# Performance work log

Hardware: AMD Instinct MI355X
Metric: run time of the kernel (lower is better)

The kernel has to match this reference:

```python
import jax, jax.numpy as jnp
import numpy as np

EPS = 1e-8


def setup_inputs() -> dict:
    key = jax.random.key(0)
    k1, k2 = jax.random.split(key)
    N, D = 4096, 512
    x = jax.random.normal(k1, (N, D, 1, 1), dtype=jnp.float32)
    y = jax.random.normal(k2, (N, D, 1, 1), dtype=jnp.float32)
    return {"x": x, "y": y}


def reference(x, y):
    # squeeze trailing singleton spatial dims -> (N, D)
    xs = x[:, :, 0, 0]
    ys = y[:, :, 0, 0]
    # cosine similarity = normalize-then-GEMM (avoids (N,N,D) broadcast intermediate)
    xn = xs / jnp.maximum(jnp.linalg.norm(xs, axis=-1, keepdims=True), EPS)
    yn = ys / jnp.maximum(jnp.linalg.norm(ys, axis=-1, keepdims=True), EPS)
    sim = jnp.einsum("nd,md->nm", xn, yn)  # (N, N)
    n = sim.shape[0]
    # zero the diagonal, then mean over all N*N entries
    sim = sim * (1.0 - jnp.eye(n, dtype=sim.dtype))
    return jnp.mean(sim)
```

## Files before the change

kernel.cpp:

```cpp
#include <hip/hip_runtime.h>

#define NROWS 4096
#define DCOLS 512
#define NBLK  256
#define RBLK  64
#define EPSF 1e-8f
#define MAGICV 0x3C96A5D2u

__device__ __forceinline__ void st_agent(float* p, float v) {
    __hip_atomic_store(p, v, __ATOMIC_RELAXED, __HIP_MEMORY_SCOPE_AGENT);
}
__device__ __forceinline__ float ld_agent(const float* p) {
    return __hip_atomic_load(p, __ATOMIC_RELAXED, __HIP_MEMORY_SCOPE_AGENT);
}
__device__ __forceinline__ void st_flag(unsigned* p, unsigned v) {
    __hip_atomic_store(p, v, __ATOMIC_RELAXED, __HIP_MEMORY_SCOPE_AGENT);
}
__device__ __forceinline__ unsigned ld_flag(const unsigned* p) {
    return __hip_atomic_load(p, __ATOMIC_RELAXED, __HIP_MEMORY_SCOPE_AGENT);
}

__global__ __launch_bounds__(512) void cosloss_fused(const float4* __restrict__ x4,
                                                     const float4* __restrict__ y4,
                                                     float* __restrict__ partx,
                                                     float* __restrict__ party,
                                                     float* __restrict__ partd,
                                                     float* __restrict__ blockpart,
                                                     unsigned* __restrict__ flags,
                                                     unsigned* __restrict__ flag2,
                                                     float* __restrict__ out) {
    __shared__ float4 sx4[8][128];
    __shared__ float4 sy4[8][128];
    __shared__ float ldsd[8];
    __shared__ float ldsx[8][8];
    __shared__ float ldsy[8][8];

    const int t    = threadIdx.x;
    const int lane = t & 63;
    const int wave = t >> 6;

    {
        const int row0 = blockIdx.x * 16 + wave * 2;
        float4 psx0 = {0.f,0.f,0.f,0.f}, psx1 = {0.f,0.f,0.f,0.f};
        float4 psy0 = {0.f,0.f,0.f,0.f}, psy1 = {0.f,0.f,0.f,0.f};
        float pdiag = 0.f;

        #pragma unroll
        for (int r = 0; r < 2; ++r) {
            const size_t base = (size_t)(row0 + r) * (DCOLS / 4) + lane;
            const float4 x0 = x4[base];
            const float4 x1 = x4[base + 64];
            const float4 y0 = y4[base];
            const float4 y1 = y4[base + 64];

            float sxx = x0.x*x0.x + x0.y*x0.y + x0.z*x0.z + x0.w*x0.w
                      + x1.x*x1.x + x1.y*x1.y + x1.z*x1.z + x1.w*x1.w;
            float syy = y0.x*y0.x + y0.y*y0.y + y0.z*y0.z + y0.w*y0.w
                      + y1.x*y1.x + y1.y*y1.y + y1.z*y1.z + y1.w*y1.w;
            float sxy = x0.x*y0.x + x0.y*y0.y + x0.z*y0.z + x0.w*y0.w
                      + x1.x*y1.x + x1.y*y1.y + x1.z*y1.z + x1.w*y1.w;

            #pragma unroll
            for (int off = 1; off < 64; off <<= 1) {
                sxx += __shfl_xor(sxx, off, 64);
                syy += __shfl_xor(syy, off, 64);
                sxy += __shfl_xor(sxy, off, 64);
            }

            const float inx = 1.0f / fmaxf(sqrtf(sxx), EPSF);
            const float iny = 1.0f / fmaxf(sqrtf(syy), EPSF);

            psx0.x += x0.x*inx; psx0.y += x0.y*inx; psx0.z += x0.z*inx; psx0.w += x0.w*inx;
            psx1.x += x1.x*inx; psx1.y += x1.y*inx; psx1.z += x1.z*inx; psx1.w += x1.w*inx;
            psy0.x += y0.x*iny; psy0.y += y0.y*iny; psy0.z += y0.z*iny; psy0.w += y0.w*iny;
            psy1.x += y1.x*iny; psy1.y += y1.y*iny; psy1.z += y1.z*iny; psy1.w += y1.w*iny;
            pdiag += sxy * inx * iny;
        }

        sx4[wave][lane]      = psx0;
        sx4[wave][64 + lane] = psx1;
        sy4[wave][lane]      = psy0;
        sy4[wave][64 + lane] = psy1;
        if (lane == 0) ldsd[wave] = pdiag;
        __syncthreads();

        const float* smx = (const float*)sx4;
        const float* smy = (const float*)sy4;
        float sxs = 0.f, sys = 0.f;
        #pragma unroll
        for (int w = 0; w < 8; ++w) {
            sxs += smx[w * 512 + t];
            sys += smy[w * 512 + t];
        }
        st_agent(&partx[(size_t)blockIdx.x * DCOLS + t], sxs);
        st_agent(&party[(size_t)blockIdx.x * DCOLS + t], sys);

        if (t == 0) {
            float d = 0.f;
            #pragma unroll
            for (int w = 0; w < 8; ++w) d += ldsd[w];
            st_agent(&partd[blockIdx.x], d);
        }
    }
    __syncthreads();
    if (t == 0) st_flag(&flags[blockIdx.x], MAGICV);

    if (blockIdx.x >= RBLK) return;

    if (t < NBLK) {
        while (ld_flag(&flags[t]) != MAGICV) { }
    }
    __syncthreads();

    {
        const int j = t & 7;
        const int r = t >> 3;
        const int c = blockIdx.x * 8 + j;

        float d = (t < 4) ? ld_agent(&partd[blockIdx.x * 4 + t]) : 0.f;

        float sx = 0.f, sy = 0.f;
        #pragma unroll
        for (int i = 0; i < 4; ++i) {
            const size_t idx = (size_t)(r + 64 * i) * DCOLS + c;
            sx += ld_agent(&partx[idx]);
            sy += ld_agent(&party[idx]);
        }
        #pragma unroll
        for (int m = 8; m < 64; m <<= 1) {
            sx += __shfl_xor(sx, m, 64);
            sy += __shfl_xor(sy, m, 64);
        }
        if (lane < 8) {
            ldsx[wave][lane] = sx;
            ldsy[wave][lane] = sy;
        }
        __syncthreads();

        if (wave == 0) {
            float vx = ldsx[lane >> 3][lane & 7];
            float vy = ldsy[lane >> 3][lane & 7];
            #pragma unroll
            for (int m = 8; m < 64; m <<= 1) {
                vx += __shfl_xor(vx, m, 64);
                vy += __shfl_xor(vy, m, 64);
            }
            float v = vx * vy;
            #pragma unroll
            for (int m = 1; m < 8; m <<= 1)
                v += __shfl_xor(v, m, 64);
            #pragma unroll
            for (int m = 1; m < 4; m <<= 1)
                d += __shfl_xor(d, m, 64);
            if (lane == 0) st_agent(&blockpart[blockIdx.x], v - d);
        }
    }
    __syncthreads();
    if (t == 0) st_flag(&flag2[blockIdx.x], MAGICV);

    if (blockIdx.x != 0) return;

    if (t < RBLK) {
        while (ld_flag(&flag2[t]) != MAGICV) { }
    }
    __syncthreads();

    if (wave == 0) {
        float v = ld_agent(&blockpart[lane]);
        #pragma unroll
        for (int off = 1; off < 64; off <<= 1)
            v += __shfl_xor(v, off, 64);
        if (lane == 0) out[0] = v / 16777216.0f;
    }
}

extern "C" void kernel_launch(void* const* d_in, const int* in_sizes, int n_in,
                              void* d_out, int out_size, void* d_ws, size_t ws_size,
                              hipStream_t stream) {
    const float4* x4 = (const float4*)d_in[0];
    const float4* y4 = (const float4*)d_in[1];
    float* out = (float*)d_out;

    float* partx      = (float*)d_ws;
    float* party      = partx + (size_t)NBLK * DCOLS;
    float* partd      = party + (size_t)NBLK * DCOLS;
    float* blockpart  = partd + NBLK;
    unsigned* flags   = (unsigned*)(blockpart + RBLK);
    unsigned* flag2   = flags + NBLK;

    cosloss_fused<<<NBLK, 512, 0, stream>>>(x4, y4, partx, party, partd,
                                            blockpart, flags, flag2, out);
}
```

Baseline: 12.49 us.

## Use half-wave rows with DPP reductions and single-wave flag polling

Each half-wave now owns one full row (16 rows per block instead of two rows per wave), and the cross-lane norm sums use DPP/swizzle folds instead of 64-lane shuffles. The normalized x and y partial sums are staged through one shared buffer in two passes. Flag waiting now uses a single wave that polls all flags with __all instead of 256 threads spinning. The aim is to cut reduction latency and spin contention, at the cost of extra barriers and LDS round trips.

Result: faster. 11.47 us (-8.1%).

```diff
diff --git a/kernel.cpp b/kernel.cpp
--- a/kernel.cpp
+++ b/kernel.cpp
@@ -18,6 +18,35 @@
 }
 __device__ __forceinline__ unsigned ld_flag(const unsigned* p) {
     return __hip_atomic_load(p, __ATOMIC_RELAXED, __HIP_MEMORY_SCOPE_AGENT);
+}
+
+template <int CTRL>
+__device__ __forceinline__ float dpp_fold(float v) {
+    union { float f; int i; } u, r;
+    u.f = v;
+    r.i = __builtin_amdgcn_update_dpp(0, u.i, CTRL, 0xF, 0xF, true);
+    return v + r.f;
+}
+__device__ __forceinline__ float swz16_fold(float v) {
+    union { float f; int i; } u, r;
+    u.f = v;
+    r.i = __builtin_amdgcn_ds_swizzle(u.i, 0x401F);
+    return v + r.f;
+}
+__device__ __forceinline__ float reduce32(float v) {
+    v = dpp_fold<0xB1>(v);
+    v = dpp_fold<0x4E>(v);
+    v = dpp_fold<0x141>(v);
+    v = dpp_fold<0x140>(v);
+    v = swz16_fold(v);
+    return v;
+}
+
+__device__ __forceinline__ float dot4(const float4 a, const float4 b) {
+    return a.x*b.x + a.y*b.y + a.z*b.z + a.w*b.w;
+}
+__device__ __forceinline__ float4 scale4(const float4 a, const float s) {
+    return make_float4(a.x*s, a.y*s, a.z*s, a.w*s);
 }
 
 __global__ __launch_bounds__(512) void cosloss_fused(const float4* __restrict__ x4,
@@ -29,76 +58,81 @@
                                                      unsigned* __restrict__ flags,
                                                      unsigned* __restrict__ flag2,
                                                      float* __restrict__ out) {
-    __shared__ float4 sx4[8][128];
-    __shared__ float4 sy4[8][128];
-    __shared__ float ldsd[8];
+    __shared__ float4 sm[16][128];
+    __shared__ float ldsd[16];
     __shared__ float ldsx[8][8];
     __shared__ float ldsy[8][8];
 
     const int t    = threadIdx.x;
     const int lane = t & 63;
     const int wave = t >> 6;
-
-    {
-        const int row0 = blockIdx.x * 16 + wave * 2;
-        float4 psx0 = {0.f,0.f,0.f,0.f}, psx1 = {0.f,0.f,0.f,0.f};
-        float4 psy0 = {0.f,0.f,0.f,0.f}, psy1 = {0.f,0.f,0.f,0.f};
-        float pdiag = 0.f;
-
-        #pragma unroll
-        for (int r = 0; r < 2; ++r) {
-            const size_t base = (size_t)(row0 + r) * (DCOLS / 4) + lane;
-            const float4 x0 = x4[base];
-            const float4 x1 = x4[base + 64];
-            const float4 y0 = y4[base];
-            const float4 y1 = y4[base + 64];
-
-            float sxx = x0.x*x0.x + x0.y*x0.y + x0.z*x0.z + x0.w*x0.w
-                      + x1.x*x1.x + x1.y*x1.y + x1.z*x1.z + x1.w*x1.w;
-            float syy = y0.x*y0.x + y0.y*y0.y + y0.z*y0.z + y0.w*y0.w
-                      + y1.x*y1.x + y1.y*y1.y + y1.z*y1.z + y1.w*y1.w;
-            float sxy = x0.x*y0.x + x0.y*y0.y + x0.z*y0.z + x0.w*y0.w
-                      + x1.x*y1.x + x1.y*y1.y + x1.z*y1.z + x1.w*y1.w;
-
-            #pragma unroll
-            for (int off = 1; off < 64; off <<= 1) {
-                sxx += __shfl_xor(sxx, off, 64);
-                syy += __shfl_xor(syy, off, 64);
-                sxy += __shfl_xor(sxy, off, 64);
-            }
-
-            const float inx = 1.0f / fmaxf(sqrtf(sxx), EPSF);
-            const float iny = 1.0f / fmaxf(sqrtf(syy), EPSF);
-
-            psx0.x += x0.x*inx; psx0.y += x0.y*inx; psx0.z += x0.z*inx; psx0.w += x0.w*inx;
-            psx1.x += x1.x*inx; psx1.y += x1.y*inx; psx1.z += x1.z*inx; psx1.w += x1.w*inx;
-            psy0.x += y0.x*iny; psy0.y += y0.y*iny; psy0.z += y0.z*iny; psy0.w += y0.w*iny;
-            psy1.x += y1.x*iny; psy1.y += y1.y*iny; psy1.z += y1.z*iny; psy1.w += y1.w*iny;
-            pdiag += sxy * inx * iny;
-        }
-
-        sx4[wave][lane]      = psx0;
-        sx4[wave][64 + lane] = psx1;
-        sy4[wave][lane]      = psy0;
-        sy4[wave][64 + lane] = psy1;
-        if (lane == 0) ldsd[wave] = pdiag;
-        __syncthreads();
-
-        const float* smx = (const float*)sx4;
-        const float* smy = (const float*)sy4;
-        float sxs = 0.f, sys = 0.f;
-        #pragma unroll
-        for (int w = 0; w < 8; ++w) {
-            sxs += smx[w * 512 + t];
-            sys += smy[w * 512 + t];
-        }
-        st_agent(&partx[(size_t)blockIdx.x * DCOLS + t], sxs);
-        st_agent(&party[(size_t)blockIdx.x * DCOLS + t], sys);
-
+    const int h    = lane >> 5;
+    const int c    = lane & 31;
+    const int g    = wave * 2 + h;
+
+    float4 b0, b1, b2, b3;
+
+    {
+        const int row = blockIdx.x * 16 + g;
+        const float4* xb = x4 + (size_t)row * (DCOLS / 4);
+        const float4* yb = y4 + (size_t)row * (DCOLS / 4);
+        const float4 xv0 = xb[c];
+        const float4 xv1 = xb[c + 32];
+        const float4 xv2 = xb[c + 64];
+        const float4 xv3 = xb[c + 96];
+        const float4 yv0 = yb[c];
+        const float4 yv1 = yb[c + 32];
+        const float4 yv2 = yb[c + 64];
+        const float4 yv3 = yb[c + 96];
+
+        float sxx = dot4(xv0,xv0) + dot4(xv1,xv1) + dot4(xv2,xv2) + dot4(xv3,xv3);
+        float syy = dot4(yv0,yv0) + dot4(yv1,yv1) + dot4(yv2,yv2) + dot4(yv3,yv3);
+        float sxy = dot4(xv0,yv0) + dot4(xv1,yv1) + dot4(xv2,yv2) + dot4(xv3,yv3);
+
+        sxx = reduce32(sxx);
+        syy = reduce32(syy);
+        sxy = reduce32(sxy);
+
+        const float inx = 1.0f / fmaxf(sqrtf(sxx), EPSF);
+        const float iny = 1.0f / fmaxf(sqrtf(syy), EPSF);
+
+        sm[g][c]      = scale4(xv0, inx);
+        sm[g][c + 32] = scale4(xv1, inx);
+        sm[g][c + 64] = scale4(xv2, inx);
+        sm[g][c + 96] = scale4(xv3, inx);
+        b0 = scale4(yv0, iny);
+        b1 = scale4(yv1, iny);
+        b2 = scale4(yv2, iny);
+        b3 = scale4(yv3, iny);
+        if (c == 0) ldsd[g] = sxy * inx * iny;
+    }
+    __syncthreads();
+
+    {
+        const float* smf = (const float*)sm;
+        float s = 0.f;
+        #pragma unroll
+        for (int gg = 0; gg < 16; ++gg) s += smf[gg * 512 + t];
+        st_agent(&partx[(size_t)blockIdx.x * DCOLS + t], s);
+    }
+    __syncthreads();
+
+    sm[g][c]      = b0;
+    sm[g][c + 32] = b1;
+    sm[g][c + 64] = b2;
+    sm[g][c + 96] = b3;
+    __syncthreads();
+
+    {
+        const float* smf = (const float*)sm;
+        float s = 0.f;
+        #pragma unroll
+        for (int gg = 0; gg < 16; ++gg) s += smf[gg * 512 + t];
+        st_agent(&party[(size_t)blockIdx.x * DCOLS + t], s);
         if (t == 0) {
             float d = 0.f;
             #pragma unroll
-            for (int w = 0; w < 8; ++w) d += ldsd[w];
+            for (int gg = 0; gg < 16; ++gg) d += ldsd[gg];
             st_agent(&partd[blockIdx.x], d);
         }
     }
@@ -107,22 +141,28 @@
 
     if (blockIdx.x >= RBLK) return;
 
-    if (t < NBLK) {
-        while (ld_flag(&flags[t]) != MAGICV) { }
+    if (wave == 0) {
+        for (;;) {
+            const bool ok = (ld_flag(&flags[lane])       == MAGICV) &
+                            (ld_flag(&flags[lane + 64])  == MAGICV) &
+                            (ld_flag(&flags[lane + 128]) == MAGICV) &
+                            (ld_flag(&flags[lane + 192]) == MAGICV);
+            if (__all(ok)) break;
+        }
     }
     __syncthreads();
 
     {
         const int j = t & 7;
         const int r = t >> 3;
-        const int c = blockIdx.x * 8 + j;
+        const int col = blockIdx.x * 8 + j;
 
         float d = (t < 4) ? ld_agent(&partd[blockIdx.x * 4 + t]) : 0.f;
 
         float sx = 0.f, sy = 0.f;
         #pragma unroll
         for (int i = 0; i < 4; ++i) {
-            const size_t idx = (size_t)(r + 64 * i) * DCOLS + c;
+            const size_t idx = (size_t)(r + 64 * i) * DCOLS + col;
             sx += ld_agent(&partx[idx]);
             sy += ld_agent(&party[idx]);
         }
@@ -160,12 +200,10 @@
 
     if (blockIdx.x != 0) return;
 
-    if (t < RBLK) {
-        while (ld_flag(&flag2[t]) != MAGICV) { }
-    }
-    __syncthreads();
-
     if (wave == 0) {
+        for (;;) {
+            if (__all(ld_flag(&flag2[lane]) == MAGICV)) break;
+        }
         float v = ld_agent(&blockpart[lane]);
         #pragma unroll
         for (int off = 1; off < 64; off <<= 1)
```
